# Kernel tuning notes

Hardware: AMD Instinct MI355X
Metric: run time of the kernel (lower is better)

## Reference

```python
import jax, jax.numpy as jnp
import numpy as np

FEATURES = 4096
BATCH = 2048


def setup_inputs() -> dict:
    key = jax.random.key(0)
    kx, kk = jax.random.split(key)
    x = jax.random.normal(kx, (BATCH, FEATURES), dtype=jnp.float32)
    kernel = jax.random.normal(kk, (FEATURES,), dtype=jnp.float32)
    return {"x": x, "kernel": kernel}


def reference(x, kernel):
    n = kernel.shape[0]
    i = jnp.arange(n)[:, None]   # [n,1]
    j = jnp.arange(n)[None, :]   # [1,n]
    idx = i - j                   # Toeplitz offsets
    # W[i,j] = kernel[i-j] if i>=j else 0  (causal lower-triangular Toeplitz)
    W = jnp.where(idx >= 0, kernel[jnp.clip(idx, 0, n - 1)], 0.0)
    # out[b,i] = sum_{j<=i} x[b,j] * kernel[i-j]  == x @ W.T
    return x @ W.T
```

## Files before the change

kernel.cpp:

```cpp
#include <hip/hip_runtime.h>
#include <hip/hip_bf16.h>


typedef unsigned short u16;
typedef __attribute__((ext_vector_type(8))) short  bf16x8;
typedef __attribute__((ext_vector_type(8))) unsigned short u16x8;
typedef __attribute__((ext_vector_type(4))) float  f32x4;

#define KDIM 4096
#define NDIM 4096
#define MDIM 2048
#define KREV_STRIDE 4608
#define KREV_BYTES  (8 * KREV_STRIDE * 2)
#define BSTRIDE 456
#define BBUF    (8 * BSTRIDE)

#define MFMA_BF16 __builtin_amdgcn_mfma_f32_16x16x32_bf16

static __device__ inline u16 f2bf(float f) {
  unsigned u = __builtin_bit_cast(unsigned, f);
  unsigned r = u + 0x7FFFu + ((u >> 16) & 1u);
  return (u16)(r >> 16);
}

static __device__ inline void async_copy16(const void* g, void* l) {
  __builtin_amdgcn_global_load_lds((const __attribute__((address_space(1))) void*)g,
                                   (__attribute__((address_space(3))) void*)l,
                                   16, 0, 0);
}

__global__ __launch_bounds__(256) void prep(const float* __restrict__ x,
                                            const float* __restrict__ kern,
                                            u16* __restrict__ xb,
                                            u16* __restrict__ krevs,
                                            int conv_blocks) {
  int kblk = (int)blockIdx.x - conv_blocks;
  if (kblk >= 0) {
    int u = kblk * 256 + threadIdx.x;
    for (int a = 0; a < 8; ++a) {
      int t = u + a - 8;
      u16 v = 0;
      if (t >= 0 && t <= 4095) v = f2bf(kern[4095 - t]);
      krevs[a * KREV_STRIDE + u] = v;
    }
  } else {
    unsigned tg  = blockIdx.x * 256 + threadIdx.x;
    unsigned l   = tg & 63;
    unsigned kb  = (tg >> 6) & 127;
    unsigned rg  = tg >> 13;
    unsigned row = rg * 16 + (l & 15);
    unsigned k   = kb * 32 + (l >> 4) * 8;
    const f32x4* p = (const f32x4*)(x + (size_t)row * KDIM + k);
    f32x4 v0 = p[0], v1 = p[1];
    u16x8 r;
    r[0] = f2bf(v0[0]); r[1] = f2bf(v0[1]); r[2] = f2bf(v0[2]); r[3] = f2bf(v0[3]);
    r[4] = f2bf(v1[0]); r[5] = f2bf(v1[1]); r[6] = f2bf(v1[2]); r[7] = f2bf(v1[3]);
    *(u16x8*)(xb + (size_t)tg * 8) = r;
  }
}

template <bool CONV>
__global__ __launch_bounds__(512, 4) void toeplitz_gemm(const void* __restrict__ Av,
                                                        const u16* __restrict__ krevs,
                                                        float* __restrict__ out) {
  __shared__ __align__(16) char smem_raw[36864];
  u16*   B_all = (u16*)smem_raw;
  f32x4* ep    = (f32x4*)smem_raw;

  const int tid  = threadIdx.x;
  const int w    = tid >> 6;
  const int g    = w >> 2;
  const int wl   = w & 3;
  const int lane = tid & 63;
  const int lane16 = lane & 15;
  const int quad   = lane >> 4;
  const int wm = wl >> 1;
  const int wn = wl & 1;

  const int b  = (int)blockIdx.x;
  const int x_ = b & 7;
  const int jj = b >> 3;
  const int q  = jj & 31;
  const int h  = jj >> 5;
  const int mt = x_ + 8 * (q & 1);
  const int ct = h ? (q >> 1) : 31 - (q >> 1);
  const int n0 = ct * 128;
  const int m0 = mt * 128;
  const int W  = 3968 - n0;

  int boff[4];
  for (int fn = 0; fn < 4; ++fn) {
    int n_g = n0 + wn * 64 + fn * 16 + lane16;
    int s0  = 4095 - n_g + quad * 8;
    int a   = s0 & 7;
    boff[fn] = a * BSTRIDE + (s0 - a + 8 - W);
  }

  f32x4 acc[4][4] = {};

  const u16*   xb2 = (const u16*)Av;
  const float* xf  = (const float*)Av;
  const u16* pA[4];
  if constexpr (!CONV) {
    for (int fm = 0; fm < 4; ++fm)
      pA[fm] = xb2 + (size_t)(mt * 8 + wm * 4 + fm) * 65536 + g * 1024 + lane * 8;
  }
  const int rowb = m0 + wm * 64 + lane16;

  auto stageB = [&](int c) {
    if (lane < 56)
      async_copy16(krevs + w * KREV_STRIDE + W + c * 256 + (lane << 3),
                   &B_all[(c & 1) * BBUF + w * BSTRIDE]);
  };

  stageB(0);
  asm volatile("s_waitcnt vmcnt(0) lgkmcnt(0)" ::: "memory");
  __builtin_amdgcn_s_barrier();
  asm volatile("" ::: "memory");

  const int cmax = ct >> 1;
  for (int t = 0; ; ++t) {
    if (!(t & 1) && ((t >> 1) + 1) <= cmax) stageB((t >> 1) + 1);

    const u16* Bb  = B_all + ((t >> 1) & 1) * BBUF;
    const int  ksl = (t & 1) * 128 + g * 64;
#pragma unroll
    for (int kk = 0; kk < 2; ++kk) {
      bf16x8 af[4];
      if constexpr (!CONV) {
        const int eo = t * 2048 + kk * 512;
        for (int fm = 0; fm < 4; ++fm)
          af[fm] = *(const bf16x8*)(pA[fm] + eo);
      } else {
        const int k0 = t * 128 + g * 64 + kk * 32 + quad * 8;
        for (int fm = 0; fm < 4; ++fm) {
          const f32x4* px = (const f32x4*)(xf + (size_t)(rowb + fm * 16) * KDIM + k0);
          f32x4 v0 = px[0], v1 = px[1];
          u16x8 r;
          r[0]=f2bf(v0[0]); r[1]=f2bf(v0[1]); r[2]=f2bf(v0[2]); r[3]=f2bf(v0[3]);
          r[4]=f2bf(v1[0]); r[5]=f2bf(v1[1]); r[6]=f2bf(v1[2]); r[7]=f2bf(v1[3]);
          af[fm] = __builtin_bit_cast(bf16x8, r);
        }
      }
      bf16x8 bfr[4];
      for (int fn = 0; fn < 4; ++fn)
        bfr[fn] = *(const bf16x8*)(&Bb[boff[fn] + ksl + kk * 32]);
      for (int fm = 0; fm < 4; ++fm)
        for (int fn = 0; fn < 4; ++fn)
          acc[fm][fn] = MFMA_BF16(af[fm], bfr[fn], acc[fm][fn], 0, 0, 0);
    }
    if (t == ct) break;
    if (t & 1) {
      asm volatile("s_waitcnt vmcnt(0) lgkmcnt(0)" ::: "memory");
      __builtin_amdgcn_s_barrier();
      asm volatile("" ::: "memory");
    }
  }

  const int j = tid & 255;
  for (int r = 0; r < 2; ++r) {
    __syncthreads();
    if (g == 1) {
      for (int fm2 = 0; fm2 < 2; ++fm2)
        for (int fn = 0; fn < 4; ++fn)
          ep[j * 9 + fm2 * 4 + fn] = acc[r * 2 + fm2][fn];
    }
    __syncthreads();
    if (g == 0) {
      for (int fm2 = 0; fm2 < 2; ++fm2)
        for (int fn = 0; fn < 4; ++fn)
          acc[r * 2 + fm2][fn] += ep[j * 9 + fm2 * 4 + fn];
    }
  }

  if (g == 0) {
    for (int fm = 0; fm < 4; ++fm) {
      int row_base = m0 + wm * 64 + fm * 16 + quad * 4;
      for (int fn = 0; fn < 4; ++fn) {
        int col = n0 + wn * 64 + fn * 16 + lane16;
        for (int r = 0; r < 4; ++r)
          out[(size_t)(row_base + r) * NDIM + col] = acc[fm][fn][r];
      }
    }
  }
}

extern "C" void kernel_launch(void* const* d_in, const int* in_sizes, int n_in,
                              void* d_out, int out_size, void* d_ws, size_t ws_size,
                              hipStream_t stream) {
  const float* x    = (const float*)d_in[0];
  const float* kern = (const float*)d_in[1];
  float* out = (float*)d_out;

  u16* krevs = (u16*)d_ws;
  u16* xb    = (u16*)((char*)d_ws + KREV_BYTES);
  const size_t need_fast = (size_t)KREV_BYTES + (size_t)MDIM * KDIM * 2;

  if (ws_size >= need_fast) {
    prep<<<4096 + 18, 256, 0, stream>>>(x, kern, xb, krevs, 4096);
    toeplitz_gemm<false><<<512, 512, 0, stream>>>(xb, krevs, out);
  } else {
    prep<<<18, 256, 0, stream>>>(x, kern, xb, krevs, 0);
    toeplitz_gemm<true><<<512, 512, 0, stream>>>(x, krevs, out);
  }
}
```

Baseline: 124.8 us.

## Stage A tiles through swizzled LDS ring with async loads instead of fragment-layout global reads

The prep kernel now writes bf16 x in plain row-major order instead of a pre-swizzled MFMA fragment layout. The GEMM stages A tiles into a triple-buffered, XOR-swizzled LDS ring using async global-to-LDS copies with fine-grained vmcnt waits, and each wave reads its MFMA fragments from LDS. The aim is to overlap A loads with MFMA work and make the global loads coalesced row-wise. In exchange, LDS use rises to about 62KB per block, which may limit occupancy, and the loop now has more LDS traffic and barriers.

```diff
diff --git a/kernel.cpp b/kernel.cpp
--- a/kernel.cpp
+++ b/kernel.cpp
@@ -14,6 +14,7 @@
 #define KREV_BYTES  (8 * KREV_STRIDE * 2)
 #define BSTRIDE 456
 #define BBUF    (8 * BSTRIDE)
+#define ABUFS   49152
 
 #define MFMA_BF16 __builtin_amdgcn_mfma_f32_16x16x32_bf16
 
@@ -34,9 +35,9 @@
                                             u16* __restrict__ xb,
                                             u16* __restrict__ krevs,
                                             int conv_blocks) {
-  int kblk = (int)blockIdx.x - conv_blocks;
-  if (kblk >= 0) {
-    int u = kblk * 256 + threadIdx.x;
+  int kb = (int)blockIdx.x - conv_blocks;
+  if (kb >= 0) {
+    int u = kb * 256 + threadIdx.x;
     for (int a = 0; a < 8; ++a) {
       int t = u + a - 8;
       u16 v = 0;
@@ -44,18 +45,13 @@
       krevs[a * KREV_STRIDE + u] = v;
     }
   } else {
-    unsigned tg  = blockIdx.x * 256 + threadIdx.x;
-    unsigned l   = tg & 63;
-    unsigned kb  = (tg >> 6) & 127;
-    unsigned rg  = tg >> 13;
-    unsigned row = rg * 16 + (l & 15);
-    unsigned k   = kb * 32 + (l >> 4) * 8;
-    const f32x4* p = (const f32x4*)(x + (size_t)row * KDIM + k);
+    size_t i = ((size_t)blockIdx.x * 256 + threadIdx.x) * 8;
+    const f32x4* p = (const f32x4*)(x + i);
     f32x4 v0 = p[0], v1 = p[1];
     u16x8 r;
     r[0] = f2bf(v0[0]); r[1] = f2bf(v0[1]); r[2] = f2bf(v0[2]); r[3] = f2bf(v0[3]);
     r[4] = f2bf(v1[0]); r[5] = f2bf(v1[1]); r[6] = f2bf(v1[2]); r[7] = f2bf(v1[3]);
-    *(u16x8*)(xb + (size_t)tg * 8) = r;
+    *(u16x8*)(xb + i) = r;
   }
 }
 
@@ -63,8 +59,8 @@
 __global__ __launch_bounds__(512, 4) void toeplitz_gemm(const void* __restrict__ Av,
                                                         const u16* __restrict__ krevs,
                                                         float* __restrict__ out) {
-  __shared__ __align__(16) char smem_raw[36864];
-  u16*   B_all = (u16*)smem_raw;
+  __shared__ __align__(16) char smem_raw[63744];
+  u16*   B_all = (u16*)(smem_raw + ABUFS);
   f32x4* ep    = (f32x4*)smem_raw;
 
   const int tid  = threadIdx.x;
@@ -81,12 +77,14 @@
   const int x_ = b & 7;
   const int jj = b >> 3;
   const int q  = jj & 31;
-  const int h  = jj >> 5;
+  const int h2 = jj >> 5;
   const int mt = x_ + 8 * (q & 1);
-  const int ct = h ? (q >> 1) : 31 - (q >> 1);
+  const int ct = h2 ? (q >> 1) : 31 - (q >> 1);
   const int n0 = ct * 128;
   const int m0 = mt * 128;
   const int W  = 3968 - n0;
+  const int hmax = 2 * ct + 1;
+  const int cmax = ct >> 1;
 
   int boff[4];
   for (int fn = 0; fn < 4; ++fn) {
@@ -98,62 +96,90 @@
 
   f32x4 acc[4][4] = {};
 
-  const u16*   xb2 = (const u16*)Av;
-  const float* xf  = (const float*)Av;
-  const u16* pA[4];
-  if constexpr (!CONV) {
-    for (int fm = 0; fm < 4; ++fm)
-      pA[fm] = xb2 + (size_t)(mt * 8 + wm * 4 + fm) * 65536 + g * 1024 + lane * 8;
-  }
-  const int rowb = m0 + wm * 64 + lane16;
-
+  const int u_   = (lane & 7) ^ ((lane >> 3) & 7);
+  const int srow = 2 * (lane >> 3) + (u_ >> 2);
+  const int skof = (u_ & 3) * 8;
+  const int aoff = wm * 4096 + (lane16 >> 1) * 128 +
+                   ((((lane16 & 1) << 2) | quad) ^ (lane16 >> 1)) * 16;
+
+  const u16*   xb = (const u16*)Av;
+  const float* xf = (const float*)Av;
+  char* Agrp = smem_raw + g * 8192;
+
+  const u16* srcbase = xb + (size_t)(m0 + wm * 64 + srow) * KDIM + g * 32 + skof;
+
+  auto stageA = [&](int hh, int ss) {
+    char* dst = Agrp + ss * 16384 + wm * 4096;
+    const u16* sp = srcbase + (size_t)hh * 64;
+    for (int c = 0; c < 4; ++c)
+      async_copy16(sp + (size_t)c * 16 * KDIM, dst + c * 1024);
+  };
+  auto stageA_conv = [&](int hh, int ss) {
+    char* dst = Agrp + ss * 16384 + wm * 4096;
+    for (int c = 0; c < 4; ++c) {
+      const float* px = xf + (size_t)(m0 + wm * 64 + c * 16 + srow) * KDIM +
+                        (size_t)hh * 64 + g * 32 + skof;
+      f32x4 v0 = *(const f32x4*)px, v1 = *(const f32x4*)(px + 4);
+      u16x8 r;
+      r[0]=f2bf(v0[0]); r[1]=f2bf(v0[1]); r[2]=f2bf(v0[2]); r[3]=f2bf(v0[3]);
+      r[4]=f2bf(v1[0]); r[5]=f2bf(v1[1]); r[6]=f2bf(v1[2]); r[7]=f2bf(v1[3]);
+      *(u16x8*)(dst + c * 1024 + lane * 16) = r;
+    }
+  };
   auto stageB = [&](int c) {
     if (lane < 56)
       async_copy16(krevs + w * KREV_STRIDE + W + c * 256 + (lane << 3),
                    &B_all[(c & 1) * BBUF + w * BSTRIDE]);
   };
 
-  stageB(0);
-  asm volatile("s_waitcnt vmcnt(0) lgkmcnt(0)" ::: "memory");
-  __builtin_amdgcn_s_barrier();
-  asm volatile("" ::: "memory");
-
-  const int cmax = ct >> 1;
-  for (int t = 0; ; ++t) {
-    if (!(t & 1) && ((t >> 1) + 1) <= cmax) stageB((t >> 1) + 1);
-
-    const u16* Bb  = B_all + ((t >> 1) & 1) * BBUF;
-    const int  ksl = (t & 1) * 128 + g * 64;
-#pragma unroll
-    for (int kk = 0; kk < 2; ++kk) {
-      bf16x8 af[4];
-      if constexpr (!CONV) {
-        const int eo = t * 2048 + kk * 512;
-        for (int fm = 0; fm < 4; ++fm)
-          af[fm] = *(const bf16x8*)(pA[fm] + eo);
-      } else {
-        const int k0 = t * 128 + g * 64 + kk * 32 + quad * 8;
-        for (int fm = 0; fm < 4; ++fm) {
-          const f32x4* px = (const f32x4*)(xf + (size_t)(rowb + fm * 16) * KDIM + k0);
-          f32x4 v0 = px[0], v1 = px[1];
-          u16x8 r;
-          r[0]=f2bf(v0[0]); r[1]=f2bf(v0[1]); r[2]=f2bf(v0[2]); r[3]=f2bf(v0[3]);
-          r[4]=f2bf(v1[0]); r[5]=f2bf(v1[1]); r[6]=f2bf(v1[2]); r[7]=f2bf(v1[3]);
-          af[fm] = __builtin_bit_cast(bf16x8, r);
-        }
+  auto compute = [&](int hh, int ss) {
+    const u16* Bb  = B_all + ((hh >> 2) & 1) * BBUF;
+    const int bofs = (hh & 3) * 64 + g * 32;
+    const char* Ab = Agrp + ss * 16384;
+    bf16x8 af[4], bfr[4];
+    for (int fm = 0; fm < 4; ++fm)
+      af[fm] = *(const bf16x8*)(Ab + aoff + fm * 1024);
+    for (int fn = 0; fn < 4; ++fn)
+      bfr[fn] = *(const bf16x8*)(&Bb[boff[fn] + bofs]);
+    for (int fm = 0; fm < 4; ++fm)
+      for (int fn = 0; fn < 4; ++fn)
+        acc[fm][fn] = MFMA_BF16(af[fm], bfr[fn], acc[fm][fn], 0, 0, 0);
+  };
+
+  int s = 0, sw = 1;
+  if constexpr (!CONV) {
+    stageB(0);
+    stageA(0, 0);
+    asm volatile("s_waitcnt vmcnt(0)" ::: "memory");
+    __builtin_amdgcn_s_barrier();
+    asm volatile("" ::: "memory");
+    for (int h = 0; ; ++h) {
+      int nleft = 0;
+      if ((h & 3) == 0 && (h >> 2) + 1 <= cmax) { stageB((h >> 2) + 1); nleft += 1; }
+      if (h + 1 <= hmax) { stageA(h + 1, sw); nleft += 4; }
+      if (nleft == 5)      asm volatile("s_waitcnt vmcnt(5)" ::: "memory");
+      else if (nleft == 4) asm volatile("s_waitcnt vmcnt(4)" ::: "memory");
+      else                 asm volatile("s_waitcnt vmcnt(0)" ::: "memory");
+      compute(h, s);
+      if (h == hmax) break;
+      if (h & 1) {
+        asm volatile("" ::: "memory");
+        __builtin_amdgcn_s_barrier();
+        asm volatile("" ::: "memory");
       }
-      bf16x8 bfr[4];
-      for (int fn = 0; fn < 4; ++fn)
-        bfr[fn] = *(const bf16x8*)(&Bb[boff[fn] + ksl + kk * 32]);
-      for (int fm = 0; fm < 4; ++fm)
-        for (int fn = 0; fn < 4; ++fn)
-          acc[fm][fn] = MFMA_BF16(af[fm], bfr[fn], acc[fm][fn], 0, 0, 0);
-    }
-    if (t == ct) break;
-    if (t & 1) {
-      asm volatile("s_waitcnt vmcnt(0) lgkmcnt(0)" ::: "memory");
-      __builtin_amdgcn_s_barrier();
-      asm volatile("" ::: "memory");
+      s = sw; sw = (sw == 2) ? 0 : sw + 1;
+    }
+  } else {
+    stageB(0);
+    stageA_conv(0, 0);
+    __syncthreads();
+    for (int h = 0; ; ++h) {
+      if ((h & 3) == 0 && (h >> 2) + 1 <= cmax) stageB((h >> 2) + 1);
+      compute(h, s);
+      if (h < hmax) stageA_conv(h + 1, sw);
+      if (h == hmax) break;
+      __syncthreads();
+      s = sw; sw = (sw == 2) ? 0 : sw + 1;
     }
   }
 
```

Result: no change. 125.0 us (+0.2%).

## Software-pipeline A fragment loads one step ahead with partial vmcnt waits

Applied to the files above, without the earlier changes.

In the prepacked-bf16 path, A fragments for the next k-step are now prefetched into registers (two register sets, one per k half) while the current step's MFMAs run. Barrier waits use vmcnt(12)/vmcnt(8) instead of draining all loads, so outstanding A prefetches stay in flight across the B-buffer barrier. B fragments are loaded one column at a time and wave-uniform indices are moved to scalar registers. The aim is to hide global A-load latency behind MFMA work, at the cost of more registers and hand-counted vmcnt values whose correctness depends on the compiler's load ordering.

```diff
diff --git a/kernel.cpp b/kernel.cpp
--- a/kernel.cpp
+++ b/kernel.cpp
@@ -81,12 +81,13 @@
   const int x_ = b & 7;
   const int jj = b >> 3;
   const int q  = jj & 31;
-  const int h  = jj >> 5;
+  const int h2 = jj >> 5;
   const int mt = x_ + 8 * (q & 1);
-  const int ct = h ? (q >> 1) : 31 - (q >> 1);
+  const int ct = h2 ? (q >> 1) : 31 - (q >> 1);
   const int n0 = ct * 128;
   const int m0 = mt * 128;
   const int W  = 3968 - n0;
+  const int cmax = ct >> 1;
 
   int boff[4];
   for (int fn = 0; fn < 4; ++fn) {
@@ -98,62 +99,101 @@
 
   f32x4 acc[4][4] = {};
 
+  const int wmu = __builtin_amdgcn_readfirstlane(wm);
+  const int gu  = __builtin_amdgcn_readfirstlane(g);
   const u16*   xb2 = (const u16*)Av;
   const float* xf  = (const float*)Av;
-  const u16* pA[4];
-  if constexpr (!CONV) {
-    for (int fm = 0; fm < 4; ++fm)
-      pA[fm] = xb2 + (size_t)(mt * 8 + wm * 4 + fm) * 65536 + g * 1024 + lane * 8;
-  }
+  int aoffs[4];
+  for (int fm = 0; fm < 4; ++fm)
+    aoffs[fm] = (mt * 8 + wmu * 4 + fm) * 65536 + gu * 1024 + lane * 8;
   const int rowb = m0 + wm * 64 + lane16;
 
+  auto ldA = [&](int fm, int t, int kk) -> bf16x8 {
+    return *(const bf16x8*)(xb2 + aoffs[fm] + t * 2048 + kk * 512);
+  };
+  auto ldAc = [&](int fm, int t, int kk) -> bf16x8 {
+    const float* px = xf + (size_t)(rowb + fm * 16) * KDIM +
+                      t * 128 + gu * 64 + kk * 32 + quad * 8;
+    f32x4 v0 = *(const f32x4*)px, v1 = *(const f32x4*)(px + 4);
+    u16x8 r;
+    r[0]=f2bf(v0[0]); r[1]=f2bf(v0[1]); r[2]=f2bf(v0[2]); r[3]=f2bf(v0[3]);
+    r[4]=f2bf(v1[0]); r[5]=f2bf(v1[1]); r[6]=f2bf(v1[2]); r[7]=f2bf(v1[3]);
+    return __builtin_bit_cast(bf16x8, r);
+  };
   auto stageB = [&](int c) {
     if (lane < 56)
       async_copy16(krevs + w * KREV_STRIDE + W + c * 256 + (lane << 3),
                    &B_all[(c & 1) * BBUF + w * BSTRIDE]);
   };
 
-  stageB(0);
-  asm volatile("s_waitcnt vmcnt(0) lgkmcnt(0)" ::: "memory");
-  __builtin_amdgcn_s_barrier();
-  asm volatile("" ::: "memory");
-
-  const int cmax = ct >> 1;
-  for (int t = 0; ; ++t) {
-    if (!(t & 1) && ((t >> 1) + 1) <= cmax) stageB((t >> 1) + 1);
-
-    const u16* Bb  = B_all + ((t >> 1) & 1) * BBUF;
-    const int  ksl = (t & 1) * 128 + g * 64;
-#pragma unroll
-    for (int kk = 0; kk < 2; ++kk) {
-      bf16x8 af[4];
-      if constexpr (!CONV) {
-        const int eo = t * 2048 + kk * 512;
+  if constexpr (!CONV) {
+    bf16x8 afA[4], afB[4];
+    stageB(0);
+#pragma unroll
+    for (int fm = 0; fm < 4; ++fm) afA[fm] = ldA(fm, 0, 0);
+#pragma unroll
+    for (int fm = 0; fm < 4; ++fm) afB[fm] = ldA(fm, 0, 1);
+    asm volatile("s_waitcnt vmcnt(8)" ::: "memory");
+    __builtin_amdgcn_s_barrier();
+    asm volatile("" ::: "memory");
+
+    for (int t = 0; ; ++t) {
+      const u16* Bb  = B_all + ((t >> 1) & 1) * BBUF;
+      const int  ksl = (t & 1) * 128 + g * 64;
+#pragma unroll
+      for (int fn = 0; fn < 4; ++fn) {
+        bf16x8 bv = *(const bf16x8*)(&Bb[boff[fn] + ksl]);
+#pragma unroll
         for (int fm = 0; fm < 4; ++fm)
-          af[fm] = *(const bf16x8*)(pA[fm] + eo);
-      } else {
-        const int k0 = t * 128 + g * 64 + kk * 32 + quad * 8;
-        for (int fm = 0; fm < 4; ++fm) {
-          const f32x4* px = (const f32x4*)(xf + (size_t)(rowb + fm * 16) * KDIM + k0);
-          f32x4 v0 = px[0], v1 = px[1];
-          u16x8 r;
-          r[0]=f2bf(v0[0]); r[1]=f2bf(v0[1]); r[2]=f2bf(v0[2]); r[3]=f2bf(v0[3]);
-          r[4]=f2bf(v1[0]); r[5]=f2bf(v1[1]); r[6]=f2bf(v1[2]); r[7]=f2bf(v1[3]);
-          af[fm] = __builtin_bit_cast(bf16x8, r);
+          acc[fm][fn] = MFMA_BF16(afA[fm], bv, acc[fm][fn], 0, 0, 0);
+      }
+      if (t < ct)
+#pragma unroll
+        for (int fm = 0; fm < 4; ++fm) afA[fm] = ldA(fm, t + 1, 0);
+      if (!(t & 1) && (t >> 1) + 1 <= cmax) stageB((t >> 1) + 1);
+#pragma unroll
+      for (int fn = 0; fn < 4; ++fn) {
+        bf16x8 bv = *(const bf16x8*)(&Bb[boff[fn] + ksl + 32]);
+#pragma unroll
+        for (int fm = 0; fm < 4; ++fm)
+          acc[fm][fn] = MFMA_BF16(afB[fm], bv, acc[fm][fn], 0, 0, 0);
+      }
+      if (t < ct)
+#pragma unroll
+        for (int fm = 0; fm < 4; ++fm) afB[fm] = ldA(fm, t + 1, 1);
+      if (t == ct) break;
+      if (t & 1) {
+        asm volatile("s_waitcnt vmcnt(12)" ::: "memory");
+        __builtin_amdgcn_s_barrier();
+        asm volatile("" ::: "memory");
+      }
+    }
+  } else {
+    stageB(0);
+    asm volatile("s_waitcnt vmcnt(0)" ::: "memory");
+    __syncthreads();
+    for (int t = 0; ; ++t) {
+      const u16* Bb  = B_all + ((t >> 1) & 1) * BBUF;
+      const int  ksl = (t & 1) * 128 + g * 64;
+      if (!(t & 1) && (t >> 1) + 1 <= cmax) stageB((t >> 1) + 1);
+#pragma unroll
+      for (int kk = 0; kk < 2; ++kk) {
+        bf16x8 af[4];
+#pragma unroll
+        for (int fm = 0; fm < 4; ++fm) af[fm] = ldAc(fm, t, kk);
+#pragma unroll
+        for (int fn = 0; fn < 4; ++fn) {
+          bf16x8 bv = *(const bf16x8*)(&Bb[boff[fn] + ksl + kk * 32]);
+#pragma unroll
+          for (int fm = 0; fm < 4; ++fm)
+            acc[fm][fn] = MFMA_BF16(af[fm], bv, acc[fm][fn], 0, 0, 0);
         }
       }
-      bf16x8 bfr[4];
-      for (int fn = 0; fn < 4; ++fn)
-        bfr[fn] = *(const bf16x8*)(&Bb[boff[fn] + ksl + kk * 32]);
-      for (int fm = 0; fm < 4; ++fm)
-        for (int fn = 0; fn < 4; ++fn)
-          acc[fm][fn] = MFMA_BF16(af[fm], bfr[fn], acc[fm][fn], 0, 0, 0);
-    }
-    if (t == ct) break;
-    if (t & 1) {
-      asm volatile("s_waitcnt vmcnt(0) lgkmcnt(0)" ::: "memory");
-      __builtin_amdgcn_s_barrier();
-      asm volatile("" ::: "memory");
+      if (t == ct) break;
+      if (t & 1) {
+        asm volatile("s_waitcnt vmcnt(0)" ::: "memory");
+        __syncthreads();
+      }
     }
   }
 
```

Result: faster. 122.2 us (-2.1%).
